# Performance work log

Measured on AMD Instinct MI355X. Metric: run time of the kernel, lower is better.

## Reference

```python
import jax, jax.numpy as jnp
import numpy as np

N_HEAD = 8
PREFIX_LEN = 77  # hardcoded text prefix length in the 'prefix' model_type branch
MASKED_BIAS = -10000.0


def setup_inputs() -> dict:
    key = jax.random.key(0)
    k1, k2, k3 = jax.random.split(key, 3)
    B, S, D = 8, 1024, 1024
    x = jax.random.normal(k1, (B, S, D), dtype=jnp.float32)
    attention_mask = jnp.zeros((B, 1, 1, S), dtype=jnp.float32)
    W_attn = jax.random.normal(k2, (D, 3 * D), dtype=jnp.float32) * 0.02
    b_attn = jnp.zeros((3 * D,), dtype=jnp.float32)
    W_proj = jax.random.normal(k3, (D, D), dtype=jnp.float32) * 0.02
    b_proj = jnp.zeros((D,), dtype=jnp.float32)
    return {"x": x, "attention_mask": attention_mask, "W_attn": W_attn,
            "b_attn": b_attn, "W_proj": W_proj, "b_proj": b_proj}


def _prefix_mask(S):
    # Rows < 77: attend only to cols < 77 (bidirectional prefix).
    # Rows >= 77: standard causal (cols <= row).
    row = jnp.arange(S)[:, None]
    col = jnp.arange(S)[None, :]
    return jnp.where(row < PREFIX_LEN, col < PREFIX_LEN, col <= row)  # [S, S] bool


def reference(x, attention_mask, W_attn, b_attn, W_proj, b_proj):
    B, S, D = x.shape
    H = N_HEAD
    hd = D // H
    qkv = x @ W_attn + b_attn                         # [B, S, 3D]
    q, k, v = jnp.split(qkv, 3, axis=-1)
    q = q.reshape(B, S, H, hd).transpose(0, 2, 1, 3)  # [B, H, S, hd]
    k = k.reshape(B, S, H, hd).transpose(0, 2, 1, 3)
    v = v.reshape(B, S, H, hd).transpose(0, 2, 1, 3)
    w = jnp.einsum('bhqd,bhkd->bhqk', q, k) / jnp.sqrt(jnp.float32(hd))
    mask = _prefix_mask(S)[None, None]                # [1, 1, S, S]
    w = jnp.where(mask, w, jnp.float32(MASKED_BIAS))
    w = w + attention_mask                            # additive mask [B,1,1,S]
    w = jax.nn.softmax(w, axis=-1)
    # dropout omitted (eval-mode reference)
    a = jnp.einsum('bhqk,bhkd->bhqd', w, v)           # [B, H, S, hd]
    a = a.transpose(0, 2, 1, 3).reshape(B, S, D)      # merge heads
    return a @ W_proj + b_proj
```

## Files before the change

kernel.cpp:

```cpp
#include <hip/hip_runtime.h>
#include <cstdint>
#include <cstddef>

#define B_  8
#define S_  1024
#define D_  1024
#define H_  8
#define HD_ 128
#define N3_ 3072
#define PREFIX 77
#define MASKED_BIAS -10000.0f

typedef __bf16 bf16x8 __attribute__((ext_vector_type(8)));
typedef float  f32x4  __attribute__((ext_vector_type(4)));

__device__ __forceinline__ unsigned short f2bf_rne(float f) {
    unsigned int u = __float_as_uint(f);
    u += 0x7FFFu + ((u >> 16) & 1u);
    return (unsigned short)(u >> 16);
}
__device__ __forceinline__ float bf2f(unsigned short h) {
    return __uint_as_float(((unsigned int)h) << 16);
}

__device__ __forceinline__ void load_lds16(const unsigned short* g, unsigned short* l) {
    __builtin_amdgcn_global_load_lds(
        (const __attribute__((address_space(1))) unsigned int*)g,
        (__attribute__((address_space(3))) unsigned int*)l,
        16, 0, 0);
}

__global__ void prep(const float* __restrict__ x, unsigned short* __restrict__ xb,
                     const float* __restrict__ Wa, unsigned short* __restrict__ wta,
                     const float* __restrict__ Wp, unsigned short* __restrict__ wph) {
    __shared__ float tile[32][33];
    const int bid = (int)blockIdx.x;
    const int tid = threadIdx.x;
    if (bid < 8192) {
        const int i = bid * 256 + tid;
        float4 v = reinterpret_cast<const float4*>(x)[i];
        ushort4 o;
        o.x = f2bf_rne(v.x); o.y = f2bf_rne(v.y); o.z = f2bf_rne(v.z); o.w = f2bf_rne(v.w);
        reinterpret_cast<ushort4*>(xb)[i] = o;
        return;
    }
    const float* in; unsigned short* out; int C, bx, by;
    if (bid < 8192 + 3072) {
        const int lb = bid - 8192;
        in = Wa; out = wta; C = N3_;
        bx = lb % 96; by = lb / 96;
    } else {
        const int lb = bid - 11264;
        in = Wp; out = wph; C = D_;
        bx = lb & 31; by = lb >> 5;
    }
    const int c0 = bx * 32, r0 = by * 32;
    const int tx = tid & 31, ty = tid >> 5;
    #pragma unroll
    for (int i = 0; i < 4; ++i)
        tile[ty + i * 8][tx] = in[(size_t)(r0 + ty + i * 8) * C + c0 + tx];
    __syncthreads();
    #pragma unroll
    for (int i = 0; i < 4; ++i)
        out[(size_t)(c0 + ty + i * 8) * D_ + r0 + tx] = f2bf_rne(tile[tx][ty + i * 8]);
}

__global__ void transpose_v(const unsigned short* __restrict__ v, unsigned short* __restrict__ vt) {
    __shared__ unsigned short tile[32][33];
    const int bh = blockIdx.z;
    const int d0 = blockIdx.x * 32, s0 = blockIdx.y * 32;
    const unsigned short* vi = v + (size_t)bh * S_ * HD_;
    unsigned short* vo = vt + (size_t)bh * S_ * HD_;
    const int tx = threadIdx.x, ty = threadIdx.y;
    #pragma unroll
    for (int i = 0; i < 4; ++i)
        tile[ty + i * 8][tx] = vi[(size_t)(s0 + ty + i * 8) * HD_ + d0 + tx];
    __syncthreads();
    #pragma unroll
    for (int i = 0; i < 4; ++i)
        vo[(size_t)(d0 + ty + i * 8) * S_ + s0 + tx] = tile[tx][ty + i * 8];
}

__global__ __launch_bounds__(256) void gemm_qkv(
    const unsigned short* __restrict__ xb,
    const unsigned short* __restrict__ wt,
    const float* __restrict__ bias,
    unsigned short* __restrict__ qb,
    unsigned short* __restrict__ kb,
    unsigned short* __restrict__ vb) {
    __shared__ unsigned short As[128 * 32];
    __shared__ unsigned short Bs[128 * 32];
    const int tid = threadIdx.x;
    const int bid = (int)blockIdx.x;
    const int xcd = bid & 7, l = bid >> 3;
    const int m0 = (xcd * 8 + (l & 7)) * 128;
    const int n0 = (l >> 3) * 128;
    const int w = tid >> 6, lane = tid & 63;
    const int wm = (w >> 1) * 64, wn = (w & 1) * 64;
    const int l15 = lane & 15, l4 = lane >> 4;
    const int sr = lane >> 2;
    const int sc8 = ((lane & 3) ^ ((lane >> 3) & 3)) * 8;
    const unsigned short* gA0 = xb + (size_t)(m0 + w * 32 + sr) * 1024 + sc8;
    const unsigned short* gA1 = gA0 + 16 * 1024;
    const unsigned short* gB0 = wt + (size_t)(n0 + w * 32 + sr) * 1024 + sc8;
    const unsigned short* gB1 = gB0 + 16 * 1024;
    unsigned short* lA0 = As + w * 1024;
    unsigned short* lA1 = lA0 + 512;
    unsigned short* lB0 = Bs + w * 1024;
    unsigned short* lB1 = lB0 + 512;
    const int ch8 = (l4 ^ ((l15 >> 1) & 3)) * 8;
    f32x4 acc[4][4] = {};
    for (int kt = 0; kt < 32; ++kt) {
        const int k0 = kt * 32;
        __syncthreads();
        load_lds16(gA0 + k0, lA0);
        load_lds16(gA1 + k0, lA1);
        load_lds16(gB0 + k0, lB0);
        load_lds16(gB1 + k0, lB1);
        __syncthreads();
        bf16x8 af[4], bfr[4];
        #pragma unroll
        for (int i = 0; i < 4; ++i) {
            af[i]  = *(const bf16x8*)&As[(wm + i * 16 + l15) * 32 + ch8];
            bfr[i] = *(const bf16x8*)&Bs[(wn + i * 16 + l15) * 32 + ch8];
        }
        #pragma unroll
        for (int mi = 0; mi < 4; ++mi)
            #pragma unroll
            for (int ni = 0; ni < 4; ++ni)
                acc[mi][ni] = __builtin_amdgcn_mfma_f32_16x16x32_bf16(af[mi], bfr[ni], acc[mi][ni], 0, 0, 0);
    }
    #pragma unroll
    for (int mi = 0; mi < 4; ++mi) {
        #pragma unroll
        for (int ni = 0; ni < 4; ++ni) {
            const int col = n0 + wn + ni * 16 + l15;
            const float bv = bias[col];
            const int part = col >> 10;
            const int cidx = col & 1023;
            const int h = cidx >> 7, d = cidx & 127;
            unsigned short* dst = (part == 0) ? qb : ((part == 1) ? kb : vb);
            #pragma unroll
            for (int r = 0; r < 4; ++r) {
                const int row = m0 + wm + mi * 16 + l4 * 4 + r;
                const int b = row >> 10, s = row & 1023;
                dst[((size_t)(b * 8 + h) * 1024 + s) * 128 + d] = f2bf_rne(acc[mi][ni][r] + bv);
            }
        }
    }
}

__global__ __launch_bounds__(256, 2) void attn(
    const unsigned short* __restrict__ qb,
    const unsigned short* __restrict__ kb,
    const unsigned short* __restrict__ vt,
    const float* __restrict__ amask,
    unsigned short* __restrict__ ah,
    unsigned short* __restrict__ al) {
    __shared__ unsigned short Ks[2][64 * 128];
    __shared__ unsigned short Vs[128 * 64];
    __shared__ unsigned short P_lds[4][16 * 72];
    const int tid = threadIdx.x;
    const int w = tid >> 6, lane = tid & 63;
    const int l15 = lane & 15, l4 = lane >> 4;
    const int bidx = (int)blockIdx.x;
    const int qt = 15 - (bidx >> 6);
    const int h = bidx & 7, b = (bidx >> 3) & 7;
    const int bh = b * H_ + h;
    const unsigned short* Q = qb + (size_t)bh * S_ * HD_;
    const unsigned short* Kg = kb + (size_t)bh * S_ * HD_;
    const unsigned short* Vg = vt + (size_t)bh * S_ * HD_;
    unsigned short* pl = P_lds[w];
    const float L2E = 1.44269504088896341f;
    const float SCL = 0.08838834764831845f * L2E;
    const float M2  = 8.0f;

    const int q0 = qt * 64;
    const int q0w = q0 + w * 16;
    bf16x8 qf[4];
    #pragma unroll
    for (int s = 0; s < 4; ++s)
        qf[s] = *(const bf16x8*)(Q + (size_t)(q0w + l15) * 128 + s * 32 + l4 * 8);
    float lsum[4] = {0.f, 0.f, 0.f, 0.f};
    f32x4 o[8] = {};
    const int limit = (q0 + 64 > PREFIX) ? (q0 + 64) : PREFIX;
    const int nkt = (limit + 63) >> 6;

    const int kr = lane >> 4;
    const int kc = lane & 15;
    const int vr = lane >> 3;
    const int vc = lane & 7;

    #pragma unroll
    for (int j = 0; j < 4; ++j) {
        const int rl = w * 16 + j * 4 + kr;
        const int g = kc ^ (j * 4 + kr);
        load_lds16(Kg + (size_t)rl * 128 + g * 8, &Ks[0][(w * 16 + j * 4) * 128]);
    }

    for (int kt = 0; kt < nkt; ++kt) {
        const int kbase = kt * 64;
        const int cur = kt & 1;
        __syncthreads();
        if (kt + 1 < nkt) {
            const int kb2 = (kt + 1) * 64;
            #pragma unroll
            for (int j = 0; j < 4; ++j) {
                const int rl = w * 16 + j * 4 + kr;
                const int g = kc ^ (j * 4 + kr);
                load_lds16(Kg + (size_t)(kb2 + rl) * 128 + g * 8, &Ks[cur ^ 1][(w * 16 + j * 4) * 128]);
            }
        }
        #pragma unroll
        for (int j = 0; j < 4; ++j) {
            const int rv = w * 32 + j * 8 + vr;
            const int g = vc ^ vr;
            load_lds16(Vg + (size_t)rv * 1024 + kbase + g * 8, &Vs[(w * 32 + j * 8) * 64]);
        }
        const bool full = (kbase + 64 <= PREFIX) || (q0w >= PREFIX && kbase + 64 <= q0w);
        #pragma unroll
        for (int t = 0; t < 4; ++t) {
            f32x4 sa = {};
            #pragma unroll
            for (int s = 0; s < 4; ++s) {
                bf16x8 kf = *(const bf16x8*)&Ks[cur][(t * 16 + l15) * 128 + (((s * 4 + l4) ^ l15) * 8)];
                sa = __builtin_amdgcn_mfma_f32_16x16x32_bf16(qf[s], kf, sa, 0, 0, 0);
            }
            const int kcol = kbase + t * 16 + l15;
            const float am = fmaf(amask[b * S_ + kcol], L2E, -M2);
            float p[4];
            if (full) {
                #pragma unroll
                for (int r = 0; r < 4; ++r) p[r] = exp2f(fmaf(sa[r], SCL, am));
            } else {
                #pragma unroll
                for (int r = 0; r < 4; ++r) {
                    const int row = q0w + l4 * 4 + r;
                    const bool keep = (row < PREFIX) ? (kcol < PREFIX) : (kcol <= row);
                    const float e = exp2f(fmaf(sa[r], SCL, am));
                    p[r] = keep ? e : 0.f;
                }
            }
            #pragma unroll
            for (int r = 0; r < 4; ++r) {
                lsum[r] += p[r];
                pl[(l4 * 4 + r) * 72 + t * 16 + l15] = f2bf_rne(p[r]);
            }
        }
        bf16x8 pf0 = *(const bf16x8*)&pl[l15 * 72 + l4 * 8];
        bf16x8 pf1 = *(const bf16x8*)&pl[l15 * 72 + 32 + l4 * 8];
        __syncthreads();
        #pragma unroll
        for (int n = 0; n < 8; ++n) {
            bf16x8 vf = *(const bf16x8*)&Vs[(n * 16 + l15) * 64 + ((l4 ^ (l15 & 7)) * 8)];
            o[n] = __builtin_amdgcn_mfma_f32_16x16x32_bf16(pf0, vf, o[n], 0, 0, 0);
        }
        #pragma unroll
        for (int n = 0; n < 8; ++n) {
            bf16x8 vf = *(const bf16x8*)&Vs[(n * 16 + l15) * 64 + ((((4 + l4) ^ (l15 & 7))) * 8)];
            o[n] = __builtin_amdgcn_mfma_f32_16x16x32_bf16(pf1, vf, o[n], 0, 0, 0);
        }
    }
    float inv_l[4];
    #pragma unroll
    for (int r = 0; r < 4; ++r) {
        float sm = lsum[r];
        sm += __shfl_xor(sm, 1);
        sm += __shfl_xor(sm, 2);
        sm += __shfl_xor(sm, 4);
        sm += __shfl_xor(sm, 8);
        inv_l[r] = 1.0f / sm;
    }
    #pragma unroll
    for (int n = 0; n < 8; ++n) {
        const int d = n * 16 + l15;
        #pragma unroll
        for (int r = 0; r < 4; ++r) {
            const int s = q0w + l4 * 4 + r;
            const float val = o[n][r] * inv_l[r];
            const size_t idx = ((size_t)b * 1024 + s) * 1024 + h * 128 + d;
            unsigned short hv = f2bf_rne(val);
            ah[idx] = hv;
            al[idx] = f2bf_rne(val - bf2f(hv));
        }
    }
}

__global__ __launch_bounds__(256) void gemm_proj(
    const unsigned short* __restrict__ ahp,
    const unsigned short* __restrict__ alp,
    const unsigned short* __restrict__ wh,
    const float* __restrict__ bias,
    float* __restrict__ out) {
    __shared__ unsigned short As[128 * 32];
    __shared__ unsigned short Bs[128 * 32];
    const int tid = threadIdx.x;
    const int bid = (int)blockIdx.x;
    const int xcd = bid & 7, l = bid >> 3;
    const int m0 = (xcd * 8 + (l >> 3)) * 128;
    const int n0 = (l & 7) * 128;
    const int w = tid >> 6, lane = tid & 63;
    const int wm = (w >> 1) * 64, wn = (w & 1) * 64;
    const int l15 = lane & 15, l4 = lane >> 4;
    const int sr = lane >> 2;
    const int sc8 = ((lane & 3) ^ ((lane >> 3) & 3)) * 8;
    const size_t offA = (size_t)(m0 + w * 32 + sr) * 1024 + sc8;
    const size_t offB = (size_t)(n0 + w * 32 + sr) * 1024 + sc8;
    unsigned short* lA0 = As + w * 1024;
    unsigned short* lA1 = lA0 + 512;
    unsigned short* lB0 = Bs + w * 1024;
    unsigned short* lB1 = lB0 + 512;
    const int ch8 = (l4 ^ ((l15 >> 1) & 3)) * 8;
    f32x4 acc[4][4] = {};
    for (int kt = 0; kt < 64; ++kt) {
        const int seg = kt >> 5;
        const int k0 = (kt & 31) * 32;
        const unsigned short* Ap = ((seg == 1) ? alp : ahp) + offA + k0;
        const unsigned short* Bp = wh + offB + k0;
        __syncthreads();
        load_lds16(Ap, lA0);
        load_lds16(Ap + 16 * 1024, lA1);
        load_lds16(Bp, lB0);
        load_lds16(Bp + 16 * 1024, lB1);
        __syncthreads();
        bf16x8 af[4], bfr[4];
        #pragma unroll
        for (int i = 0; i < 4; ++i) {
            af[i]  = *(const bf16x8*)&As[(wm + i * 16 + l15) * 32 + ch8];
            bfr[i] = *(const bf16x8*)&Bs[(wn + i * 16 + l15) * 32 + ch8];
        }
        #pragma unroll
        for (int mi = 0; mi < 4; ++mi)
            #pragma unroll
            for (int ni = 0; ni < 4; ++ni)
                acc[mi][ni] = __builtin_amdgcn_mfma_f32_16x16x32_bf16(af[mi], bfr[ni], acc[mi][ni], 0, 0, 0);
    }
    #pragma unroll
    for (int mi = 0; mi < 4; ++mi) {
        #pragma unroll
        for (int ni = 0; ni < 4; ++ni) {
            const int col = n0 + wn + ni * 16 + l15;
            const float bv = bias[col];
            #pragma unroll
            for (int r = 0; r < 4; ++r) {
                const int row = m0 + wm + mi * 16 + l4 * 4 + r;
                out[(size_t)row * 1024 + col] = acc[mi][ni][r] + bv;
            }
        }
    }
}

extern "C" void kernel_launch(void* const* d_in, const int* in_sizes, int n_in,
                              void* d_out, int out_size, void* d_ws, size_t ws_size,
                              hipStream_t stream) {
    const float* x      = (const float*)d_in[0];
    const float* amask  = (const float*)d_in[1];
    const float* W_attn = (const float*)d_in[2];
    const float* b_attn = (const float*)d_in[3];
    const float* W_proj = (const float*)d_in[4];
    const float* b_proj = (const float*)d_in[5];
    float* out = (float*)d_out;

    char* ws = (char*)d_ws;
    unsigned short* xb  = (unsigned short*)(ws);
    unsigned short* wta = (unsigned short*)(ws + 16777216);
    unsigned short* qb  = (unsigned short*)(ws + 23068672);
    unsigned short* kb2 = (unsigned short*)(ws + 39845888);
    unsigned short* vb  = (unsigned short*)(ws + 56623104);
    unsigned short* vtb = (unsigned short*)(ws + 73400320);
    unsigned short* ahi = (unsigned short*)(ws + 90177536);
    unsigned short* alo = (unsigned short*)(ws + 106954752);
    unsigned short* wph = (unsigned short*)(ws + 123731968);

    prep<<<dim3(12288), 256, 0, stream>>>(x, xb, W_attn, wta, W_proj, wph);
    gemm_qkv<<<dim3(1536), 256, 0, stream>>>(xb, wta, b_attn, qb, kb2, vb);
    transpose_v<<<dim3(HD_ / 32, S_ / 32, B_ * H_), dim3(32, 8), 0, stream>>>(vb, vtb);
    attn<<<dim3(1024), 256, 0, stream>>>(qb, kb2, vtb, amask, ahi, alo);
    gemm_proj<<<dim3(512), 256, 0, stream>>>(ahi, alo, wph, b_proj, out);
}
```

Measured before the change: 255.3 us.

## Fuse V transpose into QKV GEMM epilogue and deepen GEMM K-tiles to 64

The QKV GEMM epilogue now writes V directly in transposed [bh, d, s] layout using 4-wide vector stores, so the separate transpose_v kernel and its extra read/write pass are removed. Both GEMMs also move from a K-tile of 32 to 64 with a new XOR swizzle, halving the number of barrier-synchronised iterations and doubling the MFMA work per LDS fill. The cost is twice the LDS per block, which may lower occupancy, and more scattered Q/K stores are unchanged.

```diff
diff --git a/kernel.cpp b/kernel.cpp
--- a/kernel.cpp
+++ b/kernel.cpp
@@ -65,31 +65,15 @@
         out[(size_t)(c0 + ty + i * 8) * D_ + r0 + tx] = f2bf_rne(tile[tx][ty + i * 8]);
 }
 
-__global__ void transpose_v(const unsigned short* __restrict__ v, unsigned short* __restrict__ vt) {
-    __shared__ unsigned short tile[32][33];
-    const int bh = blockIdx.z;
-    const int d0 = blockIdx.x * 32, s0 = blockIdx.y * 32;
-    const unsigned short* vi = v + (size_t)bh * S_ * HD_;
-    unsigned short* vo = vt + (size_t)bh * S_ * HD_;
-    const int tx = threadIdx.x, ty = threadIdx.y;
-    #pragma unroll
-    for (int i = 0; i < 4; ++i)
-        tile[ty + i * 8][tx] = vi[(size_t)(s0 + ty + i * 8) * HD_ + d0 + tx];
-    __syncthreads();
-    #pragma unroll
-    for (int i = 0; i < 4; ++i)
-        vo[(size_t)(d0 + ty + i * 8) * S_ + s0 + tx] = tile[tx][ty + i * 8];
-}
-
 __global__ __launch_bounds__(256) void gemm_qkv(
     const unsigned short* __restrict__ xb,
     const unsigned short* __restrict__ wt,
     const float* __restrict__ bias,
     unsigned short* __restrict__ qb,
     unsigned short* __restrict__ kb,
-    unsigned short* __restrict__ vb) {
-    __shared__ unsigned short As[128 * 32];
-    __shared__ unsigned short Bs[128 * 32];
+    unsigned short* __restrict__ vtb) {
+    __shared__ unsigned short As[128 * 64];
+    __shared__ unsigned short Bs[128 * 64];
     const int tid = threadIdx.x;
     const int bid = (int)blockIdx.x;
     const int xcd = bid & 7, l = bid >> 3;
@@ -98,37 +82,39 @@
     const int w = tid >> 6, lane = tid & 63;
     const int wm = (w >> 1) * 64, wn = (w & 1) * 64;
     const int l15 = lane & 15, l4 = lane >> 4;
-    const int sr = lane >> 2;
-    const int sc8 = ((lane & 3) ^ ((lane >> 3) & 3)) * 8;
-    const unsigned short* gA0 = xb + (size_t)(m0 + w * 32 + sr) * 1024 + sc8;
-    const unsigned short* gA1 = gA0 + 16 * 1024;
-    const unsigned short* gB0 = wt + (size_t)(n0 + w * 32 + sr) * 1024 + sc8;
-    const unsigned short* gB1 = gB0 + 16 * 1024;
-    unsigned short* lA0 = As + w * 1024;
-    unsigned short* lA1 = lA0 + 512;
-    unsigned short* lB0 = Bs + w * 1024;
-    unsigned short* lB1 = lB0 + 512;
-    const int ch8 = (l4 ^ ((l15 >> 1) & 3)) * 8;
+    const int sr = lane >> 3;
+    const int sc8 = ((lane & 7) ^ sr) * 8;
+    const unsigned short* gA = xb + (size_t)(m0 + w * 32 + sr) * 1024 + sc8;
+    const unsigned short* gB = wt + (size_t)(n0 + w * 32 + sr) * 1024 + sc8;
+    unsigned short* lA = As + w * 32 * 64;
+    unsigned short* lB = Bs + w * 32 * 64;
     f32x4 acc[4][4] = {};
-    for (int kt = 0; kt < 32; ++kt) {
-        const int k0 = kt * 32;
-        __syncthreads();
-        load_lds16(gA0 + k0, lA0);
-        load_lds16(gA1 + k0, lA1);
-        load_lds16(gB0 + k0, lB0);
-        load_lds16(gB1 + k0, lB1);
-        __syncthreads();
-        bf16x8 af[4], bfr[4];
-        #pragma unroll
-        for (int i = 0; i < 4; ++i) {
-            af[i]  = *(const bf16x8*)&As[(wm + i * 16 + l15) * 32 + ch8];
-            bfr[i] = *(const bf16x8*)&Bs[(wn + i * 16 + l15) * 32 + ch8];
-        }
-        #pragma unroll
-        for (int mi = 0; mi < 4; ++mi)
-            #pragma unroll
-            for (int ni = 0; ni < 4; ++ni)
-                acc[mi][ni] = __builtin_amdgcn_mfma_f32_16x16x32_bf16(af[mi], bfr[ni], acc[mi][ni], 0, 0, 0);
+    for (int kt = 0; kt < 16; ++kt) {
+        const int k0 = kt * 64;
+        __syncthreads();
+        #pragma unroll
+        for (int j = 0; j < 4; ++j) {
+            load_lds16(gA + k0 + j * 8 * 1024, lA + j * 512);
+            load_lds16(gB + k0 + j * 8 * 1024, lB + j * 512);
+        }
+        __syncthreads();
+        bf16x8 af[2][4], bfr[2][4];
+        #pragma unroll
+        for (int kk = 0; kk < 2; ++kk) {
+            #pragma unroll
+            for (int i = 0; i < 4; ++i) {
+                const int cha = ((kk * 4 + l4) ^ (l15 & 7)) * 8;
+                af[kk][i]  = *(const bf16x8*)&As[(wm + i * 16 + l15) * 64 + cha];
+                bfr[kk][i] = *(const bf16x8*)&Bs[(wn + i * 16 + l15) * 64 + cha];
+            }
+        }
+        #pragma unroll
+        for (int kk = 0; kk < 2; ++kk)
+            #pragma unroll
+            for (int mi = 0; mi < 4; ++mi)
+                #pragma unroll
+                for (int ni = 0; ni < 4; ++ni)
+                    acc[mi][ni] = __builtin_amdgcn_mfma_f32_16x16x32_bf16(af[kk][mi], bfr[kk][ni], acc[mi][ni], 0, 0, 0);
     }
     #pragma unroll
     for (int mi = 0; mi < 4; ++mi) {
@@ -139,12 +125,20 @@
             const int part = col >> 10;
             const int cidx = col & 1023;
             const int h = cidx >> 7, d = cidx & 127;
-            unsigned short* dst = (part == 0) ? qb : ((part == 1) ? kb : vb);
-            #pragma unroll
-            for (int r = 0; r < 4; ++r) {
-                const int row = m0 + wm + mi * 16 + l4 * 4 + r;
-                const int b = row >> 10, s = row & 1023;
-                dst[((size_t)(b * 8 + h) * 1024 + s) * 128 + d] = f2bf_rne(acc[mi][ni][r] + bv);
+            const int row0 = m0 + wm + mi * 16 + l4 * 4;
+            const int b = row0 >> 10, s0r = row0 & 1023;
+            if (part == 2) {
+                ushort4 vv;
+                vv.x = f2bf_rne(acc[mi][ni][0] + bv);
+                vv.y = f2bf_rne(acc[mi][ni][1] + bv);
+                vv.z = f2bf_rne(acc[mi][ni][2] + bv);
+                vv.w = f2bf_rne(acc[mi][ni][3] + bv);
+                *(ushort4*)&vtb[((size_t)(b * 8 + h) * 128 + d) * 1024 + s0r] = vv;
+            } else {
+                unsigned short* dst = part ? kb : qb;
+                #pragma unroll
+                for (int r = 0; r < 4; ++r)
+                    dst[((size_t)(b * 8 + h) * 1024 + (s0r + r)) * 128 + d] = f2bf_rne(acc[mi][ni][r] + bv);
             }
         }
     }
@@ -292,8 +286,8 @@
     const unsigned short* __restrict__ wh,
     const float* __restrict__ bias,
     float* __restrict__ out) {
-    __shared__ unsigned short As[128 * 32];
-    __shared__ unsigned short Bs[128 * 32];
+    __shared__ unsigned short As[128 * 64];
+    __shared__ unsigned short Bs[128 * 64];
     const int tid = threadIdx.x;
     const int bid = (int)blockIdx.x;
     const int xcd = bid & 7, l = bid >> 3;
@@ -302,38 +296,44 @@
     const int w = tid >> 6, lane = tid & 63;
     const int wm = (w >> 1) * 64, wn = (w & 1) * 64;
     const int l15 = lane & 15, l4 = lane >> 4;
-    const int sr = lane >> 2;
-    const int sc8 = ((lane & 3) ^ ((lane >> 3) & 3)) * 8;
+    const int sr = lane >> 3;
+    const int sc8 = ((lane & 7) ^ sr) * 8;
     const size_t offA = (size_t)(m0 + w * 32 + sr) * 1024 + sc8;
     const size_t offB = (size_t)(n0 + w * 32 + sr) * 1024 + sc8;
-    unsigned short* lA0 = As + w * 1024;
-    unsigned short* lA1 = lA0 + 512;
-    unsigned short* lB0 = Bs + w * 1024;
-    unsigned short* lB1 = lB0 + 512;
-    const int ch8 = (l4 ^ ((l15 >> 1) & 3)) * 8;
+    const unsigned short* gAh = ahp + offA;
+    const unsigned short* gAl = alp + offA;
+    const unsigned short* gB  = wh + offB;
+    unsigned short* lA = As + w * 32 * 64;
+    unsigned short* lB = Bs + w * 32 * 64;
     f32x4 acc[4][4] = {};
-    for (int kt = 0; kt < 64; ++kt) {
-        const int seg = kt >> 5;
-        const int k0 = (kt & 31) * 32;
-        const unsigned short* Ap = ((seg == 1) ? alp : ahp) + offA + k0;
-        const unsigned short* Bp = wh + offB + k0;
-        __syncthreads();
-        load_lds16(Ap, lA0);
-        load_lds16(Ap + 16 * 1024, lA1);
-        load_lds16(Bp, lB0);
-        load_lds16(Bp + 16 * 1024, lB1);
-        __syncthreads();
-        bf16x8 af[4], bfr[4];
-        #pragma unroll
-        for (int i = 0; i < 4; ++i) {
-            af[i]  = *(const bf16x8*)&As[(wm + i * 16 + l15) * 32 + ch8];
-            bfr[i] = *(const bf16x8*)&Bs[(wn + i * 16 + l15) * 32 + ch8];
-        }
-        #pragma unroll
-        for (int mi = 0; mi < 4; ++mi)
-            #pragma unroll
-            for (int ni = 0; ni < 4; ++ni)
-                acc[mi][ni] = __builtin_amdgcn_mfma_f32_16x16x32_bf16(af[mi], bfr[ni], acc[mi][ni], 0, 0, 0);
+    for (int kt = 0; kt < 32; ++kt) {
+        const int k0 = (kt & 15) * 64;
+        const unsigned short* Ap = ((kt & 16) ? gAl : gAh) + k0;
+        const unsigned short* Bp = gB + k0;
+        __syncthreads();
+        #pragma unroll
+        for (int j = 0; j < 4; ++j) {
+            load_lds16(Ap + j * 8 * 1024, lA + j * 512);
+            load_lds16(Bp + j * 8 * 1024, lB + j * 512);
+        }
+        __syncthreads();
+        bf16x8 af[2][4], bfr[2][4];
+        #pragma unroll
+        for (int kk = 0; kk < 2; ++kk) {
+            #pragma unroll
+            for (int i = 0; i < 4; ++i) {
+                const int cha = ((kk * 4 + l4) ^ (l15 & 7)) * 8;
+                af[kk][i]  = *(const bf16x8*)&As[(wm + i * 16 + l15) * 64 + cha];
+                bfr[kk][i] = *(const bf16x8*)&Bs[(wn + i * 16 + l15) * 64 + cha];
+            }
+        }
+        #pragma unroll
+        for (int kk = 0; kk < 2; ++kk)
+            #pragma unroll
+            for (int mi = 0; mi < 4; ++mi)
+                #pragma unroll
+                for (int ni = 0; ni < 4; ++ni)
+                    acc[mi][ni] = __builtin_amdgcn_mfma_f32_16x16x32_bf16(af[kk][mi], bfr[kk][ni], acc[mi][ni], 0, 0, 0);
     }
     #pragma unroll
     for (int mi = 0; mi < 4; ++mi) {
@@ -366,15 +366,13 @@
     unsigned short* wta = (unsigned short*)(ws + 16777216);
     unsigned short* qb  = (unsigned short*)(ws + 23068672);
     unsigned short* kb2 = (unsigned short*)(ws + 39845888);
-    unsigned short* vb  = (unsigned short*)(ws + 56623104);
     unsigned short* vtb = (unsigned short*)(ws + 73400320);
     unsigned short* ahi = (unsigned short*)(ws + 90177536);
     unsigned short* alo = (unsigned short*)(ws + 106954752);
     unsigned short* wph = (unsigned short*)(ws + 123731968);
 
     prep<<<dim3(12288), 256, 0, stream>>>(x, xb, W_attn, wta, W_proj, wph);
-    gemm_qkv<<<dim3(1536), 256, 0, stream>>>(xb, wta, b_attn, qb, kb2, vb);
-    transpose_v<<<dim3(HD_ / 32, S_ / 32, B_ * H_), dim3(32, 8), 0, stream>>>(vb, vtb);
+    gemm_qkv<<<dim3(1536), 256, 0, stream>>>(xb, wta, b_attn, qb, kb2, vtb);
     attn<<<dim3(1024), 256, 0, stream>>>(qb, kb2, vtb, amask, ahi, alo);
     gemm_proj<<<dim3(512), 256, 0, stream>>>(ahi, alo, wph, b_proj, out);
 }
```

New measurement: 252.0 us. No clear change (-1.3%).
